# Kernel tuning notes

Measured on AMD Instinct MI355X. Metric: run time of the kernel, lower is better.

The kernel has to match this reference:

```python
import jax, jax.numpy as jnp
import numpy as np

D_MODEL = 1024
NUM_HEADS = 16
D_K = D_MODEL // NUM_HEADS
LOCAL_WINDOW = 3
STRIDE = 4


def strided_mask(seq_len):
    # position i attends to j iff j <= i and (i-j <= local_window or (i-j) % stride == 0)
    i = jnp.arange(seq_len)[:, None]
    j = jnp.arange(seq_len)[None, :]
    d = i - j
    return (d >= 0) & ((d <= LOCAL_WINDOW) | (d % STRIDE == 0))


def setup_inputs() -> dict:
    key = jax.random.key(0)
    ks = jax.random.split(key, 11)
    B, S, D = 4, 1024, D_MODEL
    s = 1.0 / np.sqrt(D)
    inp = {
        "Q": jax.random.normal(ks[0], (B, S, D), jnp.float32),
        "K": jax.random.normal(ks[1], (B, S, D), jnp.float32),
        "V": jax.random.normal(ks[2], (B, S, D), jnp.float32),
        "Wq": jax.random.normal(ks[3], (D, D), jnp.float32) * s,
        "bq": jnp.zeros((D,), jnp.float32),
        "Wk": jax.random.normal(ks[4], (D, D), jnp.float32) * s,
        "bk": jnp.zeros((D,), jnp.float32),
        "Wv": jax.random.normal(ks[5], (D, D), jnp.float32) * s,
        "bv": jnp.zeros((D,), jnp.float32),
        "Wo": jax.random.normal(ks[6], (D, D), jnp.float32) * s,
        "bo": jnp.zeros((D,), jnp.float32),
    }
    return inp


def reference(Q, K, V, Wq, bq, Wk, bk, Wv, bv, Wo, bo):
    B, S, D = Q.shape
    H, dk = NUM_HEADS, D_K

    def split(x):  # [B,S,D] -> [B,H,S,dk]
        return x.reshape(B, S, H, dk).transpose(0, 2, 1, 3)

    q = split(Q @ Wq + bq)
    k = split(K @ Wk + bk)
    v = split(V @ Wv + bv)

    scores = jnp.einsum("bhsd,bhtd->bhst", q, k) / jnp.sqrt(
        jnp.asarray(dk, jnp.float32))
    m = strided_mask(S)[None, None]  # [1,1,S,S]
    scores = jnp.where(m, scores, -1e9)
    attn = jax.nn.softmax(scores, axis=-1)
    out = jnp.einsum("bhst,bhtd->bhsd", attn, v)
    out = out.transpose(0, 2, 1, 3).reshape(B, S, D)  # combine heads
    return out @ Wo + bo
```

## Files before the change

kernel.cpp:

```cpp
#include <hip/hip_runtime.h>

typedef _Float16 f16;
typedef __attribute__((ext_vector_type(8))) _Float16 f16x8;
typedef __attribute__((ext_vector_type(4))) _Float16 f16x4;
typedef __attribute__((ext_vector_type(4))) float f32x4;

#define MFMA16(a, b, c) __builtin_amdgcn_mfma_f32_16x16x32_f16((a), (b), (c), 0, 0, 0)

__device__ __forceinline__ void gld_lds16(const void* g, void* l) {
  __builtin_amdgcn_global_load_lds(
      (__attribute__((address_space(1))) void*)const_cast<void*>(g),
      (__attribute__((address_space(3))) void*)l, 16, 0, 0);
}

__device__ __forceinline__ f16x8 ld8(const f16* p) { return *(const f16x8*)p; }

__global__ __launch_bounds__(256) void cvt_all_kernel(
    const float* __restrict__ Q, const float* __restrict__ K, const float* __restrict__ V,
    f16* __restrict__ oq, f16* __restrict__ ok, f16* __restrict__ ov,
    const float* __restrict__ Wq, const float* __restrict__ Wk,
    const float* __restrict__ Wv, const float* __restrict__ Wo,
    f16* __restrict__ Tq, f16* __restrict__ Tk, f16* __restrict__ Tv, f16* __restrict__ To) {
  __shared__ float tile[64][65];
  if (blockIdx.z < 3) {
    const float* src = blockIdx.z == 0 ? Q : (blockIdx.z == 1 ? K : V);
    f16* dst = blockIdx.z == 0 ? oq : (blockIdx.z == 1 ? ok : ov);
    size_t i = ((size_t)blockIdx.x * 256 + threadIdx.x) * 4;
    float4 f = *(const float4*)(src + i);
    f16x4 o4;
    o4.x = (f16)f.x; o4.y = (f16)f.y; o4.z = (f16)f.z; o4.w = (f16)f.w;
    *(f16x4*)(dst + i) = o4;
    return;
  }
  if (blockIdx.x >= 1024) return;
  const int zz = blockIdx.x >> 8;
  const float* W = zz == 0 ? Wq : (zz == 1 ? Wk : (zz == 2 ? Wv : Wo));
  f16* T = zz == 0 ? Tq : (zz == 1 ? Tk : (zz == 2 ? Tv : To));
  const int tidx = blockIdx.x & 255;
  const int k0 = (tidx & 15) * 64, n0 = (tidx >> 4) * 64;
  const int tx = threadIdx.x & 63, ty = threadIdx.x >> 6;
#pragma unroll
  for (int rr = 0; rr < 16; ++rr) {
    int r = rr * 4 + ty;
    tile[r][tx] = W[(size_t)(k0 + r) * 1024 + n0 + tx];
  }
  __syncthreads();
#pragma unroll
  for (int rr = 0; rr < 16; ++rr) {
    int nn = rr * 4 + ty;
    T[(size_t)(n0 + nn) * 1024 + k0 + tx] = (f16)tile[tx][nn];
  }
}

template <bool QKV>
__global__ __launch_bounds__(256) void gemm_bt_kernel(
    const f16* __restrict__ A0, const f16* __restrict__ A1, const f16* __restrict__ A2,
    const f16* __restrict__ B0, const f16* __restrict__ B1, const f16* __restrict__ B2,
    const float* __restrict__ bias0, const float* __restrict__ bias1, const float* __restrict__ bias2,
    f16* __restrict__ C0, f16* __restrict__ C1, f16* __restrict__ C2,
    f16* __restrict__ C3, float* __restrict__ Cf) {
  const int z = blockIdx.z;
  const f16* A = z == 0 ? A0 : (z == 1 ? A1 : A2);
  const f16* Bt = z == 0 ? B0 : (z == 1 ? B1 : B2);
  const float* bias = z == 0 ? bias0 : (z == 1 ? bias1 : bias2);

  __shared__ alignas(16) f16 lA[128 * 32];
  __shared__ alignas(16) f16 lB[128 * 32];

  const int t = threadIdx.x;
  const int w = t >> 6, lane = t & 63, quad = lane >> 4, l15 = lane & 15;
  const int wm = w >> 1, wn = w & 1;
  const int mbase = blockIdx.x * 128;
  const int nbase = blockIdx.y * 128;

  const f32x4 zero4 = {0.f, 0.f, 0.f, 0.f};
  f32x4 acc[4][4];
#pragma unroll
  for (int mi = 0; mi < 4; ++mi)
#pragma unroll
    for (int ni = 0; ni < 4; ++ni) acc[mi][ni] = zero4;

  const int r = t >> 2;
  const int koff = (t & 3) * 8;

  for (int k0 = 0; k0 < 1024; k0 += 32) {
    __syncthreads();
    gld_lds16(A + (size_t)(mbase + r) * 1024 + k0 + koff, (char*)lA + w * 1024);
    gld_lds16(A + (size_t)(mbase + 64 + r) * 1024 + k0 + koff, (char*)lA + 4096 + w * 1024);
    gld_lds16(Bt + (size_t)(nbase + r) * 1024 + k0 + koff, (char*)lB + w * 1024);
    gld_lds16(Bt + (size_t)(nbase + 64 + r) * 1024 + k0 + koff, (char*)lB + 4096 + w * 1024);
    __syncthreads();

    f16x8 af[4], bf[4];
#pragma unroll
    for (int mi = 0; mi < 4; ++mi)
      af[mi] = ld8(&lA[(wm * 64 + mi * 16 + l15) * 32 + quad * 8]);
#pragma unroll
    for (int ni = 0; ni < 4; ++ni)
      bf[ni] = ld8(&lB[(wn * 64 + ni * 16 + l15) * 32 + quad * 8]);
#pragma unroll
    for (int mi = 0; mi < 4; ++mi)
#pragma unroll
      for (int ni = 0; ni < 4; ++ni)
        acc[mi][ni] = MFMA16(af[mi], bf[ni], acc[mi][ni]);
  }

#pragma unroll
  for (int mi = 0; mi < 4; ++mi) {
#pragma unroll
    for (int ni = 0; ni < 4; ++ni) {
#pragma unroll
      for (int rg = 0; rg < 4; ++rg) {
        const int row = mbase + wm * 64 + mi * 16 + quad * 4 + rg;
        const int col = nbase + wn * 64 + ni * 16 + l15;
        const float v = acc[mi][ni][rg] + bias[col];
        if (QKV) {
          const int bh = (row >> 10) * 16 + (col >> 6);
          const int s = row & 1023, d = col & 63;
          const f16 hv = (f16)v;
          if (z != 2) {
            f16* Ch = (z == 0) ? C0 : C1;
            Ch[(size_t)bh * 65536 + s * 64 + d] = hv;
          } else {
            C2[(size_t)bh * 65536 + s * 64 + d] = hv;
            const int rr = s & 3, n = s >> 2, wi = n & 63;
            C3[(size_t)bh * 65536 + (size_t)rr * 16384 + (size_t)d * 256 +
               (n & ~63) + ((wi & 15) << 2) + (wi >> 4)] = hv;
          }
        } else {
          Cf[(size_t)row * 1024 + col] = v;
        }
      }
    }
  }
}

__global__ __launch_bounds__(256) void gemm_out_kernel(
    const f16* __restrict__ A, const f16* __restrict__ Bt,
    const float* __restrict__ bias, float* __restrict__ Cf) {
  __shared__ alignas(16) f16 lA[64 * 32];
  __shared__ alignas(16) f16 lB[128 * 32];

  const int t = threadIdx.x;
  const int w = t >> 6, lane = t & 63, quad = lane >> 4, l15 = lane & 15;
  const int wm = w >> 1, wn = w & 1;
  const int mbase = blockIdx.x * 64;
  const int nbase = blockIdx.y * 128;

  const f32x4 zero4 = {0.f, 0.f, 0.f, 0.f};
  f32x4 acc[2][4];
#pragma unroll
  for (int mi = 0; mi < 2; ++mi)
#pragma unroll
    for (int ni = 0; ni < 4; ++ni) acc[mi][ni] = zero4;

  const int r = t >> 2;
  const int koff = (t & 3) * 8;

  for (int k0 = 0; k0 < 1024; k0 += 32) {
    __syncthreads();
    gld_lds16(A + (size_t)(mbase + r) * 1024 + k0 + koff, (char*)lA + w * 1024);
    gld_lds16(Bt + (size_t)(nbase + r) * 1024 + k0 + koff, (char*)lB + w * 1024);
    gld_lds16(Bt + (size_t)(nbase + 64 + r) * 1024 + k0 + koff, (char*)lB + 4096 + w * 1024);
    __syncthreads();

    f16x8 af[2], bf[4];
#pragma unroll
    for (int mi = 0; mi < 2; ++mi)
      af[mi] = ld8(&lA[(wm * 32 + mi * 16 + l15) * 32 + quad * 8]);
#pragma unroll
    for (int ni = 0; ni < 4; ++ni)
      bf[ni] = ld8(&lB[(wn * 64 + ni * 16 + l15) * 32 + quad * 8]);
#pragma unroll
    for (int mi = 0; mi < 2; ++mi)
#pragma unroll
      for (int ni = 0; ni < 4; ++ni)
        acc[mi][ni] = MFMA16(af[mi], bf[ni], acc[mi][ni]);
  }

#pragma unroll
  for (int mi = 0; mi < 2; ++mi)
#pragma unroll
    for (int ni = 0; ni < 4; ++ni)
#pragma unroll
      for (int rg = 0; rg < 4; ++rg) {
        const int row = mbase + wm * 32 + mi * 16 + quad * 4 + rg;
        const int col = nbase + wn * 64 + ni * 16 + l15;
        Cf[(size_t)row * 1024 + col] = acc[mi][ni][rg] + bias[col];
      }
}

__global__ __launch_bounds__(256) void attn_far_kernel(
    const f16* __restrict__ qh, const f16* __restrict__ kh,
    const f16* __restrict__ vtg, float* __restrict__ po, float* __restrict__ ml) {
  const int t = threadIdx.x;
  const int w = t >> 6, lane = t & 63, quad = lane >> 4, l15 = lane & 15;
  const int widx = blockIdx.x + 1024 * w;
  const int bh = (widx & 255) >> 2, r = widx & 3;
  const int wq = widx >> 8;
  const int m0 = wq * 16;
  const int ntiles = (wq >> 2) + 1;

  __shared__ alignas(16) f16 lp[4][16 * 72];

  const f16* qb = qh + (size_t)bh * 65536;
  const f16* kb = kh + (size_t)bh * 65536;
  const f16* vb = vtg + (size_t)bh * 65536 + (size_t)r * 16384;
  const float SCL2 = 0.125f * 1.44269504f;

  f16x8 aq[2];
  {
    const int i = 4 * (m0 + l15) + r;
#pragma unroll
    for (int ko = 0; ko < 2; ++ko)
      aq[ko] = ld8(qb + (size_t)i * 64 + ko * 32 + quad * 8);
  }

  const f32x4 zero4 = {0.f, 0.f, 0.f, 0.f};
  f32x4 o[4];
  float mrun[4], lrun[4];
#pragma unroll
  for (int i = 0; i < 4; ++i) {
    o[i] = zero4; mrun[i] = -1e30f; lrun[i] = 0.f;
  }

  for (int jt = 0; jt < ntiles; ++jt) {
    const int n0 = jt * 64;
    f16x8 bk0[4], bk1[4], bv0[4], bv1[4];
#pragma unroll
    for (int nt = 0; nt < 4; ++nt) {
      const f16* kr = kb + (size_t)(4 * (n0 + nt * 16 + l15) + r) * 64;
      bk0[nt] = ld8(kr + quad * 8);
      bk1[nt] = ld8(kr + 32 + quad * 8);
      const f16* vr = vb + (size_t)(nt * 16 + l15) * 256 + n0;
      bv0[nt] = ld8(vr + quad * 8);
      bv1[nt] = ld8(vr + 32 + quad * 8);
    }
    const bool lastt = (jt == ntiles - 1);
    f32x4 sc[4];
    __builtin_amdgcn_s_setprio(1);
#pragma unroll
    for (int nt = 0; nt < 4; ++nt) {
      f32x4 c = MFMA16(aq[0], bk0[nt], zero4);
      sc[nt] = MFMA16(aq[1], bk1[nt], c);
    }
    __builtin_amdgcn_s_setprio(0);
#pragma unroll
    for (int rg = 0; rg < 4; ++rg) {
      const int m = m0 + quad * 4 + rg;
      float s[4];
#pragma unroll
      for (int nt = 0; nt < 4; ++nt) {
        float vsc = sc[nt][rg] * SCL2;
        if (lastt) vsc = (n0 + nt * 16 + l15 <= m) ? vsc : -3.0e38f;
        s[nt] = vsc;
      }
      float tm = fmaxf(fmaxf(s[0], s[1]), fmaxf(s[2], s[3]));
      tm = fmaxf(tm, __shfl_xor(tm, 1));
      tm = fmaxf(tm, __shfl_xor(tm, 2));
      tm = fmaxf(tm, __shfl_xor(tm, 4));
      tm = fmaxf(tm, __shfl_xor(tm, 8));
      const float mnew = fmaxf(mrun[rg], tm);
      const float alpha = exp2f(mrun[rg] - mnew);
      float p[4], ps = 0.f;
#pragma unroll
      for (int nt = 0; nt < 4; ++nt) { p[nt] = exp2f(s[nt] - mnew); ps += p[nt]; }
      ps += __shfl_xor(ps, 1);
      ps += __shfl_xor(ps, 2);
      ps += __shfl_xor(ps, 4);
      ps += __shfl_xor(ps, 8);
      lrun[rg] = lrun[rg] * alpha + ps;
      mrun[rg] = mnew;
#pragma unroll
      for (int ntv = 0; ntv < 4; ++ntv) o[ntv][rg] *= alpha;
      f16x4 pk;
      pk.x = (f16)p[0]; pk.y = (f16)p[1]; pk.z = (f16)p[2]; pk.w = (f16)p[3];
      *(f16x4*)&lp[w][(quad * 4 + rg) * 72 + l15 * 4] = pk;
    }
    {
      const f16x8 ap0 = ld8(&lp[w][l15 * 72 + quad * 8]);
      const f16x8 ap1 = ld8(&lp[w][l15 * 72 + 32 + quad * 8]);
      __builtin_amdgcn_s_setprio(1);
#pragma unroll
      for (int ntv = 0; ntv < 4; ++ntv) {
        f32x4 c = MFMA16(ap0, bv0[ntv], o[ntv]);
        o[ntv] = MFMA16(ap1, bv1[ntv], c);
      }
      __builtin_amdgcn_s_setprio(0);
    }
  }

#pragma unroll
  for (int rg = 0; rg < 4; ++rg) {
    const int i = 4 * (m0 + quad * 4 + rg) + r;
    const size_t idx = (size_t)bh * 1024 + i;
#pragma unroll
    for (int ntv = 0; ntv < 4; ++ntv)
      po[idx * 64 + ntv * 16 + l15] = o[ntv][rg];
    if (l15 == 0) { ml[idx * 2] = mrun[rg]; ml[idx * 2 + 1] = lrun[rg]; }
  }
}

__global__ __launch_bounds__(256) void attn_diag_kernel(
    const f16* __restrict__ qh, const f16* __restrict__ kh, const f16* __restrict__ vh,
    const float* __restrict__ po, const float* __restrict__ ml, f16* __restrict__ ao) {
  const int t = threadIdx.x;
  const int w = t >> 6, lane = t & 63;
  const int ri = lane >> 3, c8 = lane & 7;
  const int g = blockIdx.x * 4 + w;
  const int bh = g >> 7;
  const int i = ((g & 127) << 3) + ri;
  const float SCL2 = 0.125f * 1.44269504f;

  const size_t rb = (size_t)bh * 65536;
  const f16x8 q8 = ld8(qh + rb + (size_t)i * 64 + c8 * 8);
  float qf[8];
#pragma unroll
  for (int e = 0; e < 8; ++e) qf[e] = (float)q8[e];

  float s[3];
  f16x8 v8[3];
#pragma unroll
  for (int d = 1; d <= 3; ++d) {
    const int j = i - d;
    const int jc = j < 0 ? 0 : j;
    const f16x8 k8 = ld8(kh + rb + (size_t)jc * 64 + c8 * 8);
    v8[d - 1] = ld8(vh + rb + (size_t)jc * 64 + c8 * 8);
    float pr = 0.f;
#pragma unroll
    for (int e = 0; e < 8; ++e) pr = fmaf(qf[e], (float)k8[e], pr);
    pr += __shfl_xor(pr, 1);
    pr += __shfl_xor(pr, 2);
    pr += __shfl_xor(pr, 4);
    s[d - 1] = (j >= 0) ? pr * SCL2 : -3.0e38f;
  }
  const float md = fmaxf(fmaxf(s[0], s[1]), s[2]);
  const size_t idx = (size_t)bh * 1024 + i;
  const float2 mlv = *(const float2*)(ml + idx * 2);
  const float mf = mlv.x, lf = mlv.y;
  const float M = fmaxf(md, mf);
  float p[3], ld = 0.f;
#pragma unroll
  for (int d = 0; d < 3; ++d) { p[d] = exp2f(s[d] - M); ld += p[d]; }
  const float fs = exp2f(mf - M);
  const float inv = 1.0f / (lf * fs + ld);
  const float4 po0 = *(const float4*)(po + idx * 64 + c8 * 8);
  const float4 po1 = *(const float4*)(po + idx * 64 + c8 * 8 + 4);
  float pe[8] = {po0.x, po0.y, po0.z, po0.w, po1.x, po1.y, po1.z, po1.w};
  f16x8 r8;
#pragma unroll
  for (int e = 0; e < 8; ++e) {
    const float ov = p[0] * (float)v8[0][e] + p[1] * (float)v8[1][e] +
                     p[2] * (float)v8[2][e];
    r8[e] = (f16)((pe[e] * fs + ov) * inv);
  }
  const int b = bh >> 4, h = bh & 15;
  *(f16x8*)(ao + ((size_t)(b * 1024 + i)) * 1024 + h * 64 + c8 * 8) = r8;
}

extern "C" void kernel_launch(void* const* d_in, const int* in_sizes, int n_in,
                              void* d_out, int out_size, void* d_ws, size_t ws_size,
                              hipStream_t stream) {
  const float* Q = (const float*)d_in[0];
  const float* K = (const float*)d_in[1];
  const float* V = (const float*)d_in[2];
  const float* Wq = (const float*)d_in[3];
  const float* bq = (const float*)d_in[4];
  const float* Wk = (const float*)d_in[5];
  const float* bk = (const float*)d_in[6];
  const float* Wv = (const float*)d_in[7];
  const float* bv = (const float*)d_in[8];
  const float* Wo = (const float*)d_in[9];
  const float* bo = (const float*)d_in[10];
  float* out = (float*)d_out;

  char* ws = (char*)d_ws;
  const size_t MB = 1ull << 20;
  f16* Xq  = (f16*)(ws + 0 * MB);
  f16* Xk  = (f16*)(ws + 8 * MB);
  f16* Xv  = (f16*)(ws + 16 * MB);
  f16* TWq = (f16*)(ws + 24 * MB);
  f16* TWk = (f16*)(ws + 26 * MB);
  f16* TWv = (f16*)(ws + 28 * MB);
  f16* TWo = (f16*)(ws + 30 * MB);
  f16* qhb = (f16*)(ws + 32 * MB);
  f16* khb = (f16*)(ws + 40 * MB);
  f16* vhb = (f16*)(ws + 48 * MB);
  f16* vtg = (f16*)(ws + 56 * MB);
  float* po  = (float*)(ws + 0 * MB);
  float* mlb = (float*)(ws + 16 * MB);
  f16* aob   = (f16*)(ws + 17 * MB);

  cvt_all_kernel<<<dim3(4096, 1, 4), 256, 0, stream>>>(
      Q, K, V, Xq, Xk, Xv, Wq, Wk, Wv, Wo, TWq, TWk, TWv, TWo);
  gemm_bt_kernel<true><<<dim3(32, 8, 3), 256, 0, stream>>>(
      Xq, Xk, Xv, TWq, TWk, TWv, bq, bk, bv, qhb, khb, vhb, vtg, nullptr);
  attn_far_kernel<<<dim3(1024), 256, 0, stream>>>(qhb, khb, vtg, po, mlb);
  attn_diag_kernel<<<dim3(2048), 256, 0, stream>>>(qhb, khb, vhb, po, mlb, aob);
  gemm_out_kernel<<<dim3(64, 8), 256, 0, stream>>>(aob, TWo, bo, out);
}
```

Measured before the change: 216.4 us.

## Fuse diagonal-window attention into far-stride kernel, dropping partial-output round trip

Merges the separate diagonal (offsets 1-3) attention kernel into the strided attention kernel. The diagonal scores are computed with MFMA and a lane shuffle to extract the diagonal, then merged with the running softmax state in registers. The fp32 partial outputs and max/sum values are no longer written to and read back from global memory, and one kernel launch is removed. The trade-off is extra per-wave work and scattered 2-byte V loads and output stores in the tail of the kernel.

Result: no change. 215.0 us (-0.7%).

```diff
diff --git a/kernel.cpp b/kernel.cpp
--- a/kernel.cpp
+++ b/kernel.cpp
@@ -190,9 +190,10 @@
       }
 }
 
-__global__ __launch_bounds__(256) void attn_far_kernel(
+__global__ __launch_bounds__(256) void attn_fused_kernel(
     const f16* __restrict__ qh, const f16* __restrict__ kh,
-    const f16* __restrict__ vtg, float* __restrict__ po, float* __restrict__ ml) {
+    const f16* __restrict__ vtg, const f16* __restrict__ vh,
+    f16* __restrict__ ao) {
   const int t = threadIdx.x;
   const int w = t >> 6, lane = t & 63, quad = lane >> 4, l15 = lane & 15;
   const int widx = blockIdx.x + 1024 * w;
@@ -290,72 +291,52 @@
     }
   }
 
+  float sd[3][4];
+#pragma unroll
+  for (int d = 1; d <= 3; ++d) {
+    f16x8 bd0, bd1;
+    {
+      int j = 4 * (m0 + l15) + r - d;
+      if (j < 0) j = 0;
+      const f16* kr = kb + (size_t)j * 64;
+      bd0 = ld8(kr + quad * 8);
+      bd1 = ld8(kr + 32 + quad * 8);
+    }
+    f32x4 c = MFMA16(aq[0], bd0, zero4);
+    c = MFMA16(aq[1], bd1, c);
+#pragma unroll
+    for (int rg = 0; rg < 4; ++rg) {
+      const float dv = __shfl(c[rg], quad * 20 + rg);
+      const int i = 4 * (m0 + quad * 4 + rg) + r;
+      sd[d - 1][rg] = (i >= d) ? dv * SCL2 : -3.0e38f;
+    }
+  }
+
+  const f16* vhb2 = vh + (size_t)bh * 65536;
+  const int b = bh >> 4, h = bh & 15;
 #pragma unroll
   for (int rg = 0; rg < 4; ++rg) {
     const int i = 4 * (m0 + quad * 4 + rg) + r;
-    const size_t idx = (size_t)bh * 1024 + i;
-#pragma unroll
-    for (int ntv = 0; ntv < 4; ++ntv)
-      po[idx * 64 + ntv * 16 + l15] = o[ntv][rg];
-    if (l15 == 0) { ml[idx * 2] = mrun[rg]; ml[idx * 2 + 1] = lrun[rg]; }
-  }
-}
-
-__global__ __launch_bounds__(256) void attn_diag_kernel(
-    const f16* __restrict__ qh, const f16* __restrict__ kh, const f16* __restrict__ vh,
-    const float* __restrict__ po, const float* __restrict__ ml, f16* __restrict__ ao) {
-  const int t = threadIdx.x;
-  const int w = t >> 6, lane = t & 63;
-  const int ri = lane >> 3, c8 = lane & 7;
-  const int g = blockIdx.x * 4 + w;
-  const int bh = g >> 7;
-  const int i = ((g & 127) << 3) + ri;
-  const float SCL2 = 0.125f * 1.44269504f;
-
-  const size_t rb = (size_t)bh * 65536;
-  const f16x8 q8 = ld8(qh + rb + (size_t)i * 64 + c8 * 8);
-  float qf[8];
-#pragma unroll
-  for (int e = 0; e < 8; ++e) qf[e] = (float)q8[e];
-
-  float s[3];
-  f16x8 v8[3];
-#pragma unroll
-  for (int d = 1; d <= 3; ++d) {
-    const int j = i - d;
-    const int jc = j < 0 ? 0 : j;
-    const f16x8 k8 = ld8(kh + rb + (size_t)jc * 64 + c8 * 8);
-    v8[d - 1] = ld8(vh + rb + (size_t)jc * 64 + c8 * 8);
-    float pr = 0.f;
-#pragma unroll
-    for (int e = 0; e < 8; ++e) pr = fmaf(qf[e], (float)k8[e], pr);
-    pr += __shfl_xor(pr, 1);
-    pr += __shfl_xor(pr, 2);
-    pr += __shfl_xor(pr, 4);
-    s[d - 1] = (j >= 0) ? pr * SCL2 : -3.0e38f;
-  }
-  const float md = fmaxf(fmaxf(s[0], s[1]), s[2]);
-  const size_t idx = (size_t)bh * 1024 + i;
-  const float2 mlv = *(const float2*)(ml + idx * 2);
-  const float mf = mlv.x, lf = mlv.y;
-  const float M = fmaxf(md, mf);
-  float p[3], ld = 0.f;
-#pragma unroll
-  for (int d = 0; d < 3; ++d) { p[d] = exp2f(s[d] - M); ld += p[d]; }
-  const float fs = exp2f(mf - M);
-  const float inv = 1.0f / (lf * fs + ld);
-  const float4 po0 = *(const float4*)(po + idx * 64 + c8 * 8);
-  const float4 po1 = *(const float4*)(po + idx * 64 + c8 * 8 + 4);
-  float pe[8] = {po0.x, po0.y, po0.z, po0.w, po1.x, po1.y, po1.z, po1.w};
-  f16x8 r8;
-#pragma unroll
-  for (int e = 0; e < 8; ++e) {
-    const float ov = p[0] * (float)v8[0][e] + p[1] * (float)v8[1][e] +
-                     p[2] * (float)v8[2][e];
-    r8[e] = (f16)((pe[e] * fs + ov) * inv);
-  }
-  const int b = bh >> 4, h = bh & 15;
-  *(f16x8*)(ao + ((size_t)(b * 1024 + i)) * 1024 + h * 64 + c8 * 8) = r8;
+    const float mdg = fmaxf(fmaxf(sd[0][rg], sd[1][rg]), sd[2][rg]);
+    const float M = fmaxf(mrun[rg], mdg);
+    const float fs = exp2f(mrun[rg] - M);
+    float p[3];
+    float ltot = lrun[rg] * fs;
+#pragma unroll
+    for (int d = 0; d < 3; ++d) { p[d] = exp2f(sd[d][rg] - M); ltot += p[d]; }
+    const float inv = 1.0f / ltot;
+    const f16* v1 = vhb2 + (size_t)((i >= 1) ? i - 1 : 0) * 64;
+    const f16* v2 = vhb2 + (size_t)((i >= 2) ? i - 2 : 0) * 64;
+    const f16* v3 = vhb2 + (size_t)((i >= 3) ? i - 3 : 0) * 64;
+    f16* aor = ao + ((size_t)(b * 1024 + i)) * 1024 + h * 64;
+#pragma unroll
+    for (int ntv = 0; ntv < 4; ++ntv) {
+      const int dc = ntv * 16 + l15;
+      const float ov = p[0] * (float)v1[dc] + p[1] * (float)v2[dc] +
+                       p[2] * (float)v3[dc];
+      aor[dc] = (f16)((o[ntv][rg] * fs + ov) * inv);
+    }
+  }
 }
 
 extern "C" void kernel_launch(void* const* d_in, const int* in_sizes, int n_in,
@@ -387,15 +368,12 @@
   f16* khb = (f16*)(ws + 40 * MB);
   f16* vhb = (f16*)(ws + 48 * MB);
   f16* vtg = (f16*)(ws + 56 * MB);
-  float* po  = (float*)(ws + 0 * MB);
-  float* mlb = (float*)(ws + 16 * MB);
-  f16* aob   = (f16*)(ws + 17 * MB);
+  f16* aob = (f16*)(ws + 17 * MB);
 
   cvt_all_kernel<<<dim3(4096, 1, 4), 256, 0, stream>>>(
       Q, K, V, Xq, Xk, Xv, Wq, Wk, Wv, Wo, TWq, TWk, TWv, TWo);
   gemm_bt_kernel<true><<<dim3(32, 8, 3), 256, 0, stream>>>(
       Xq, Xk, Xv, TWq, TWk, TWv, bq, bk, bv, qhb, khb, vhb, vtg, nullptr);
-  attn_far_kernel<<<dim3(1024), 256, 0, stream>>>(qhb, khb, vtg, po, mlb);
-  attn_diag_kernel<<<dim3(2048), 256, 0, stream>>>(qhb, khb, vhb, po, mlb, aob);
+  attn_fused_kernel<<<dim3(1024), 256, 0, stream>>>(qhb, khb, vtg, vhb, aob);
   gemm_out_kernel<<<dim3(64, 8), 256, 0, stream>>>(aob, TWo, bo, out);
 }
```
